# Optimization experiments

Measured on AMD Instinct MI355X. Metric: run time of the kernel, lower is better.

Reference implementation:

```python
import jax, jax.numpy as jnp
import numpy as np

B, D, P, K = 16384, 2048, 64, 5


def setup_inputs() -> dict:
    key = jax.random.key(0)
    k1, k2, k3, k4, k5 = jax.random.split(key, 5)
    s = 1.0 / np.sqrt(D)
    return {
        "x": jax.random.normal(k1, (B, D), dtype=jnp.float32),
        "parent_W": jax.random.normal(k2, (P, D), dtype=jnp.float32) * s,
        "parent_b": jax.random.normal(k3, (P,), dtype=jnp.float32) * s,
        "child_W": jax.random.normal(k4, (P, K, D), dtype=jnp.float32) * s,
        "child_b": jax.random.normal(k5, (P, K), dtype=jnp.float32) * s,
    }


def reference(x, parent_W, parent_b, child_W, child_b):
    # Parent linear: [B, P]
    parent_logits = x @ parent_W.T + parent_b
    # softmax is monotonic, so argmax(softmax(l)) == argmax(l)
    parent_class = jnp.argmax(parent_logits, axis=1)  # [B] int
    # Gather each sample's expert (child classifier) weights: [B, K, D], [B, K]
    Wc = child_W[parent_class]
    bc = child_b[parent_class]
    # Per-sample tiny GEMM, batched: [B, K]
    child_logits = jnp.einsum("bd,bkd->bk", x, Wc) + bc
    return parent_logits, child_logits
```

## Files before the change

kernel.cpp:

```cpp
#include <hip/hip_runtime.h>

#define B_ 16384
#define D_ 2048
#define P_ 64
#define K_ 5

#define BM 64
#define BK 64
#define KS 4
#define KSLICE (D_ / KS)
#define NCH (KSLICE / BK)

__global__ __launch_bounds__(256) void k1_parent(
    const float* __restrict__ x, const float* __restrict__ pW,
    float* __restrict__ part) {
  __shared__ float smem[BK * BM + BK * P_];
  float* xT = smem;
  float* wT = smem + BK * BM;

  const int tid = threadIdx.x;
  const int rt  = blockIdx.x & 255;
  const int ks  = blockIdx.x >> 8;
  const int b0  = rt * BM;
  const int kbase = ks * KSLICE;
  const int q   = tid & 15;
  const int rw  = tid >> 4;
  const int tc4 = (tid & 15) << 2;
  const int tr4 = (tid >> 4) << 2;

  const float* xg = x + (size_t)b0 * D_ + kbase;
  const float* wg = pW + kbase;

  float4 xa[4], wb[4];
#pragma unroll
  for (int j = 0; j < 4; ++j) {
    xa[j] = *(const float4*)&xg[(size_t)(rw + 16 * j) * D_ + (q << 2)];
    wb[j] = *(const float4*)&wg[(size_t)(rw + 16 * j) * D_ + (q << 2)];
  }

  float acc[4][4];
#pragma unroll
  for (int i = 0; i < 4; ++i)
#pragma unroll
    for (int jj = 0; jj < 4; ++jj) acc[i][jj] = 0.f;

  const int swz = q << 2;
  for (int kk = 0; kk < NCH; ++kk) {
#pragma unroll
    for (int j = 0; j < 4; ++j) {
      const int cx = (rw + 16 * j) ^ swz;
      xT[(4 * q + 0) * BM + cx] = xa[j].x;
      xT[(4 * q + 1) * BM + cx] = xa[j].y;
      xT[(4 * q + 2) * BM + cx] = xa[j].z;
      xT[(4 * q + 3) * BM + cx] = xa[j].w;
      wT[(4 * q + 0) * P_ + cx] = wb[j].x;
      wT[(4 * q + 1) * P_ + cx] = wb[j].y;
      wT[(4 * q + 2) * P_ + cx] = wb[j].z;
      wT[(4 * q + 3) * P_ + cx] = wb[j].w;
    }
    __syncthreads();
    if (kk + 1 < NCH) {
      const int d0 = (kk + 1) * BK;
#pragma unroll
      for (int j = 0; j < 4; ++j) {
        xa[j] = *(const float4*)&xg[(size_t)(rw + 16 * j) * D_ + d0 + (q << 2)];
        wb[j] = *(const float4*)&wg[(size_t)(rw + 16 * j) * D_ + d0 + (q << 2)];
      }
    }
#pragma unroll 8
    for (int d = 0; d < BK; ++d) {
      const int sz = ((d >> 2) & 15) << 2;
      const float4 xv = *(const float4*)&xT[d * BM + (tr4 ^ sz)];
      const float4 wv = *(const float4*)&wT[d * P_ + (tc4 ^ sz)];
      acc[0][0] += xv.x * wv.x; acc[0][1] += xv.x * wv.y;
      acc[0][2] += xv.x * wv.z; acc[0][3] += xv.x * wv.w;
      acc[1][0] += xv.y * wv.x; acc[1][1] += xv.y * wv.y;
      acc[1][2] += xv.y * wv.z; acc[1][3] += xv.y * wv.w;
      acc[2][0] += xv.z * wv.x; acc[2][1] += xv.z * wv.y;
      acc[2][2] += xv.z * wv.z; acc[2][3] += xv.z * wv.w;
      acc[3][0] += xv.w * wv.x; acc[3][1] += xv.w * wv.y;
      acc[3][2] += xv.w * wv.z; acc[3][3] += xv.w * wv.w;
    }
    __syncthreads();
  }

  float* po = part + (size_t)ks * (B_ * P_) + (size_t)b0 * P_;
#pragma unroll
  for (int i = 0; i < 4; ++i) {
    float4 v;
    v.x = acc[i][0]; v.y = acc[i][1]; v.z = acc[i][2]; v.w = acc[i][3];
    *(float4*)&po[(size_t)(tr4 + i) * P_ + tc4] = v;
  }
}

__global__ __launch_bounds__(256) void k_reduce(const float* __restrict__ part,
                                                const float* __restrict__ pb,
                                                float* __restrict__ pout,
                                                int* __restrict__ cnt,
                                                int* __restrict__ list) {
  const int wave = threadIdx.x >> 6, lane = threadIdx.x & 63;
  const int r = blockIdx.x * 4 + wave;
  float v = pb[lane];
#pragma unroll
  for (int s = 0; s < KS; ++s)
    v += part[(size_t)s * (B_ * P_) + (size_t)r * P_ + lane];
  pout[(size_t)r * P_ + lane] = v;

  float bv = v;
  int bi = lane;
#pragma unroll
  for (int s = 32; s > 0; s >>= 1) {
    const float ov = __shfl_xor(bv, s, 64);
    const int oi = __shfl_xor(bi, s, 64);
    if (ov > bv || (ov == bv && oi < bi)) { bv = ov; bi = oi; }
  }
  if (lane == 0) {
    const int slot = atomicAdd(&cnt[bi * 16], 1);
    if (slot < 1024) list[bi * 1024 + slot] = r;
  }
}

__global__ __launch_bounds__(256) void k2_child(const float* __restrict__ x,
                                                const float* __restrict__ cW,
                                                const float* __restrict__ cb,
                                                const int* __restrict__ cnt,
                                                const int* __restrict__ list,
                                                float* __restrict__ cout) {
  __shared__ float wlds[K_ * D_];
  const int e   = blockIdx.x >> 2;
  const int chk = blockIdx.x & 3;
  const int tid = threadIdx.x;

  const float4* wg4 = (const float4*)(cW + (size_t)e * (K_ * D_));
  float4* wl4 = (float4*)wlds;
#pragma unroll
  for (int tI = 0; tI < 10; ++tI) wl4[tid + 256 * tI] = wg4[tid + 256 * tI];
  __syncthreads();

  const int n   = min(cnt[e * 16], 1024);
  const int per = (n + 3) >> 2;
  const int lo  = chk * per;
  const int hi  = min(lo + per, n);
  const int m   = hi - lo;
  if (m <= 0) return;

  const int wave = tid >> 6, lane = tid & 63;
  const int wper = (m + 3) >> 2;
  const int wlo  = lo + wave * wper;
  const int whi  = min(wlo + wper, hi);

  const float4* x4 = (const float4*)x;
  const int* mylist = list + e * 1024;

  for (int i0 = wlo; i0 < whi; i0 += 4) {
    const int vb = min(4, whi - i0);
    const int ra = mylist[i0];
    const int rb = mylist[i0 + min(1, vb - 1)];
    const int rc = mylist[i0 + min(2, vb - 1)];
    const int rd = mylist[i0 + min(3, vb - 1)];

    float a[20];
#pragma unroll
    for (int q = 0; q < 20; ++q) a[q] = 0.f;

#pragma unroll
    for (int tt = 0; tt < 8; ++tt) {
      const float4 xv0 = x4[(size_t)ra * 512 + lane + 64 * tt];
      const float4 xv1 = x4[(size_t)rb * 512 + lane + 64 * tt];
      const float4 xv2 = x4[(size_t)rc * 512 + lane + 64 * tt];
      const float4 xv3 = x4[(size_t)rd * 512 + lane + 64 * tt];
#pragma unroll
      for (int k = 0; k < 5; ++k) {
        const float4 wv = wl4[k * 512 + lane + 64 * tt];
        a[0 * 5 + k] += xv0.x * wv.x + xv0.y * wv.y + xv0.z * wv.z + xv0.w * wv.w;
        a[1 * 5 + k] += xv1.x * wv.x + xv1.y * wv.y + xv1.z * wv.z + xv1.w * wv.w;
        a[2 * 5 + k] += xv2.x * wv.x + xv2.y * wv.y + xv2.z * wv.z + xv2.w * wv.w;
        a[3 * 5 + k] += xv3.x * wv.x + xv3.y * wv.y + xv3.z * wv.z + xv3.w * wv.w;
      }
    }
#pragma unroll
    for (int p = 0; p < 10; ++p) {
      float va = a[2 * p], vb2 = a[2 * p + 1];
      va  += __shfl_xor(va, 32, 64);
      vb2 += __shfl_xor(vb2, 32, 64);
      float z = (lane < 32) ? va : vb2;
      z += __shfl_xor(z, 16, 64);
      z += __shfl_xor(z, 8, 64);
      z += __shfl_xor(z, 4, 64);
      z += __shfl_xor(z, 2, 64);
      z += __shfl_xor(z, 1, 64);
      a[2 * p] = z;
    }
    if (lane == 0 || lane == 32) {
      const int off = (lane == 32) ? 1 : 0;
#pragma unroll
      for (int p = 0; p < 10; ++p) {
        const int f = 2 * p + off;
        const int rr = f / 5, kk = f % 5;
        if (rr < vb) {
          const int r = (rr == 0) ? ra : (rr == 1) ? rb : (rr == 2) ? rc : rd;
          cout[(size_t)r * K_ + kk] = a[2 * p] + cb[e * K_ + kk];
        }
      }
    }
  }
}

extern "C" void kernel_launch(void* const* d_in, const int* in_sizes, int n_in,
                              void* d_out, int out_size, void* d_ws, size_t ws_size,
                              hipStream_t stream) {
  const float* x  = (const float*)d_in[0];
  const float* pW = (const float*)d_in[1];
  const float* pb = (const float*)d_in[2];
  const float* cW = (const float*)d_in[3];
  const float* cb = (const float*)d_in[4];
  float* pout = (float*)d_out;
  float* cout = (float*)d_out + (size_t)B_ * P_;

  char* ws = (char*)d_ws;
  int*   cnt  = (int*)ws;
  int*   list = (int*)(ws + 4096);
  float* part = (float*)(ws + 1048576);

  hipMemsetAsync(cnt, 0, 4096, stream);
  k1_parent<<<256 * KS, 256, 0, stream>>>(x, pW, part);
  k_reduce<<<B_ / 4, 256, 0, stream>>>(part, pb, pout, cnt, list);
  k2_child<<<P_ * 4, 256, 0, stream>>>(x, cW, cb, cnt, list, cout);
}
```

Measured before the change: 267.6 us.

## Use split-fp16 MFMA for parent GEMM and fuse bias, argmax, bucketing into it

```diff
diff --git a/kernel.cpp b/kernel.cpp
--- a/kernel.cpp
+++ b/kernel.cpp
@@ -5,118 +5,153 @@
 #define P_ 64
 #define K_ 5
 
-#define BM 64
 #define BK 64
-#define KS 4
-#define KSLICE (D_ / KS)
-#define NCH (KSLICE / BK)
+#define NCH (D_ / BK)
+#define LDR 72
+#define SPLIT_SC 2048.0f
+#define SPLIT_INV (1.0f / 2048.0f)
+
+typedef _Float16 half8 __attribute__((ext_vector_type(8)));
+typedef float f32x4 __attribute__((ext_vector_type(4)));
+
+static __device__ __forceinline__ void split8(const float4 a, const float4 b,
+                                              half8& hi, half8& lo) {
+  const float v[8] = {a.x, a.y, a.z, a.w, b.x, b.y, b.z, b.w};
+#pragma unroll
+  for (int i = 0; i < 8; ++i) {
+    const _Float16 h = (_Float16)v[i];
+    hi[i] = h;
+    lo[i] = (_Float16)((v[i] - (float)h) * SPLIT_SC);
+  }
+}
 
 __global__ __launch_bounds__(256) void k1_parent(
     const float* __restrict__ x, const float* __restrict__ pW,
-    float* __restrict__ part) {
-  __shared__ float smem[BK * BM + BK * P_];
-  float* xT = smem;
-  float* wT = smem + BK * BM;
+    const float* __restrict__ pb, float* __restrict__ pout,
+    int* __restrict__ cnt, int* __restrict__ list) {
+  __shared__ _Float16 xlh[2][64 * LDR], xll[2][64 * LDR];
+  __shared__ _Float16 wlh[2][64 * LDR], wll[2][64 * LDR];
+  __shared__ float rmax[64][4];
+  __shared__ int ridx[64][4];
 
   const int tid = threadIdx.x;
-  const int rt  = blockIdx.x & 255;
-  const int ks  = blockIdx.x >> 8;
-  const int b0  = rt * BM;
-  const int kbase = ks * KSLICE;
-  const int q   = tid & 15;
-  const int rw  = tid >> 4;
-  const int tc4 = (tid & 15) << 2;
-  const int tr4 = (tid >> 4) << 2;
-
-  const float* xg = x + (size_t)b0 * D_ + kbase;
-  const float* wg = pW + kbase;
-
-  float4 xa[4], wb[4];
-#pragma unroll
-  for (int j = 0; j < 4; ++j) {
-    xa[j] = *(const float4*)&xg[(size_t)(rw + 16 * j) * D_ + (q << 2)];
-    wb[j] = *(const float4*)&wg[(size_t)(rw + 16 * j) * D_ + (q << 2)];
-  }
-
-  float acc[4][4];
-#pragma unroll
-  for (int i = 0; i < 4; ++i)
-#pragma unroll
-    for (int jj = 0; jj < 4; ++jj) acc[i][jj] = 0.f;
-
-  const int swz = q << 2;
-  for (int kk = 0; kk < NCH; ++kk) {
+  const int b0 = blockIdx.x * 64;
+  const int w = tid >> 6;
+  const int l = tid & 63;
+  const int r = tid >> 2;
+  const int c = tid & 3;
+
+  const float* xg = x + (size_t)(b0 + r) * D_ + c * 16;
+  const float* wg = pW + (size_t)r * D_ + c * 16;
+  const float bias = pb[w * 16 + (l & 15)];
+
+  const int aoff = (l & 15) * LDR + (l >> 4) * 8;
+  const int boff = (w * 16 + (l & 15)) * LDR + (l >> 4) * 8;
+  const int soff = r * LDR + c * 16;
+
+  f32x4 acc[4], accc[4];
+#pragma unroll
+  for (int fm = 0; fm < 4; ++fm) {
+    acc[fm] = {0.f, 0.f, 0.f, 0.f};
+    accc[fm] = {0.f, 0.f, 0.f, 0.f};
+  }
+
+  {
+    const float4* xp = (const float4*)xg;
+    const float4* wp = (const float4*)wg;
+    half8 h, lo;
+    split8(xp[0], xp[1], h, lo);
+    *(half8*)&xlh[0][soff] = h; *(half8*)&xll[0][soff] = lo;
+    split8(xp[2], xp[3], h, lo);
+    *(half8*)&xlh[0][soff + 8] = h; *(half8*)&xll[0][soff + 8] = lo;
+    split8(wp[0], wp[1], h, lo);
+    *(half8*)&wlh[0][soff] = h; *(half8*)&wll[0][soff] = lo;
+    split8(wp[2], wp[3], h, lo);
+    *(half8*)&wlh[0][soff + 8] = h; *(half8*)&wll[0][soff + 8] = lo;
+  }
+  __syncthreads();
+
+  for (int ch = 0; ch < NCH; ++ch) {
+    const int cur = ch & 1;
+    float4 x0, x1, x2, x3, w0, w1, w2, w3;
+    const bool more = (ch + 1 < NCH);
+    if (more) {
+      const float4* xp = (const float4*)(xg + (ch + 1) * BK);
+      const float4* wp = (const float4*)(wg + (ch + 1) * BK);
+      x0 = xp[0]; x1 = xp[1]; x2 = xp[2]; x3 = xp[3];
+      w0 = wp[0]; w1 = wp[1]; w2 = wp[2]; w3 = wp[3];
+    }
+#pragma unroll
+    for (int s = 0; s < 2; ++s) {
+      const int ko = s * 32;
+      const half8 bh = *(const half8*)&wlh[cur][boff + ko];
+      const half8 bl = *(const half8*)&wll[cur][boff + ko];
+#pragma unroll
+      for (int fm = 0; fm < 4; ++fm) {
+        const half8 ah = *(const half8*)&xlh[cur][aoff + fm * 16 * LDR + ko];
+        const half8 al = *(const half8*)&xll[cur][aoff + fm * 16 * LDR + ko];
+        acc[fm]  = __builtin_amdgcn_mfma_f32_16x16x32_f16(ah, bh, acc[fm], 0, 0, 0);
+        accc[fm] = __builtin_amdgcn_mfma_f32_16x16x32_f16(ah, bl, accc[fm], 0, 0, 0);
+        accc[fm] = __builtin_amdgcn_mfma_f32_16x16x32_f16(al, bh, accc[fm], 0, 0, 0);
+      }
+    }
+    if (more) {
+      const int nxt = cur ^ 1;
+      half8 h, lo;
+      split8(x0, x1, h, lo);
+      *(half8*)&xlh[nxt][soff] = h; *(half8*)&xll[nxt][soff] = lo;
+      split8(x2, x3, h, lo);
+      *(half8*)&xlh[nxt][soff + 8] = h; *(half8*)&xll[nxt][soff + 8] = lo;
+      split8(w0, w1, h, lo);
+      *(half8*)&wlh[nxt][soff] = h; *(half8*)&wll[nxt][soff] = lo;
+      split8(w2, w3, h, lo);
+      *(half8*)&wlh[nxt][soff + 8] = h; *(half8*)&wll[nxt][soff + 8] = lo;
+    }
+    __syncthreads();
+  }
+
+  const int colbase = w * 16 + (l & 15);
+  float val[4][4];
+#pragma unroll
+  for (int fm = 0; fm < 4; ++fm) {
 #pragma unroll
     for (int j = 0; j < 4; ++j) {
-      const int cx = (rw + 16 * j) ^ swz;
-      xT[(4 * q + 0) * BM + cx] = xa[j].x;
-      xT[(4 * q + 1) * BM + cx] = xa[j].y;
-      xT[(4 * q + 2) * BM + cx] = xa[j].z;
-      xT[(4 * q + 3) * BM + cx] = xa[j].w;
-      wT[(4 * q + 0) * P_ + cx] = wb[j].x;
-      wT[(4 * q + 1) * P_ + cx] = wb[j].y;
-      wT[(4 * q + 2) * P_ + cx] = wb[j].z;
-      wT[(4 * q + 3) * P_ + cx] = wb[j].w;
-    }
-    __syncthreads();
-    if (kk + 1 < NCH) {
-      const int d0 = (kk + 1) * BK;
-#pragma unroll
-      for (int j = 0; j < 4; ++j) {
-        xa[j] = *(const float4*)&xg[(size_t)(rw + 16 * j) * D_ + d0 + (q << 2)];
-        wb[j] = *(const float4*)&wg[(size_t)(rw + 16 * j) * D_ + d0 + (q << 2)];
-      }
-    }
-#pragma unroll 8
-    for (int d = 0; d < BK; ++d) {
-      const int sz = ((d >> 2) & 15) << 2;
-      const float4 xv = *(const float4*)&xT[d * BM + (tr4 ^ sz)];
-      const float4 wv = *(const float4*)&wT[d * P_ + (tc4 ^ sz)];
-      acc[0][0] += xv.x * wv.x; acc[0][1] += xv.x * wv.y;
-      acc[0][2] += xv.x * wv.z; acc[0][3] += xv.x * wv.w;
-      acc[1][0] += xv.y * wv.x; acc[1][1] += xv.y * wv.y;
-      acc[1][2] += xv.y * wv.z; acc[1][3] += xv.y * wv.w;
-      acc[2][0] += xv.z * wv.x; acc[2][1] += xv.z * wv.y;
-      acc[2][2] += xv.z * wv.z; acc[2][3] += xv.z * wv.w;
-      acc[3][0] += xv.w * wv.x; acc[3][1] += xv.w * wv.y;
-      acc[3][2] += xv.w * wv.z; acc[3][3] += xv.w * wv.w;
-    }
-    __syncthreads();
-  }
-
-  float* po = part + (size_t)ks * (B_ * P_) + (size_t)b0 * P_;
-#pragma unroll
-  for (int i = 0; i < 4; ++i) {
-    float4 v;
-    v.x = acc[i][0]; v.y = acc[i][1]; v.z = acc[i][2]; v.w = acc[i][3];
-    *(float4*)&po[(size_t)(tr4 + i) * P_ + tc4] = v;
-  }
-}
-
-__global__ __launch_bounds__(256) void k_reduce(const float* __restrict__ part,
-                                                const float* __restrict__ pb,
-                                                float* __restrict__ pout,
-                                                int* __restrict__ cnt,
-                                                int* __restrict__ list) {
-  const int wave = threadIdx.x >> 6, lane = threadIdx.x & 63;
-  const int r = blockIdx.x * 4 + wave;
-  float v = pb[lane];
-#pragma unroll
-  for (int s = 0; s < KS; ++s)
-    v += part[(size_t)s * (B_ * P_) + (size_t)r * P_ + lane];
-  pout[(size_t)r * P_ + lane] = v;
-
-  float bv = v;
-  int bi = lane;
-#pragma unroll
-  for (int s = 32; s > 0; s >>= 1) {
-    const float ov = __shfl_xor(bv, s, 64);
-    const int oi = __shfl_xor(bi, s, 64);
-    if (ov > bv || (ov == bv && oi < bi)) { bv = ov; bi = oi; }
-  }
-  if (lane == 0) {
+      val[fm][j] = acc[fm][j] + accc[fm][j] * SPLIT_INV + bias;
+      const int row = fm * 16 + ((l >> 4) << 2) + j;
+      pout[(size_t)(b0 + row) * P_ + colbase] = val[fm][j];
+    }
+  }
+#pragma unroll
+  for (int fm = 0; fm < 4; ++fm) {
+#pragma unroll
+    for (int j = 0; j < 4; ++j) {
+      float bv = val[fm][j];
+      int bi = colbase;
+#pragma unroll
+      for (int s = 8; s > 0; s >>= 1) {
+        const float ov = __shfl_xor(bv, s, 64);
+        const int oi = __shfl_xor(bi, s, 64);
+        if (ov > bv || (ov == bv && oi < bi)) { bv = ov; bi = oi; }
+      }
+      if ((l & 15) == 0) {
+        const int row = fm * 16 + ((l >> 4) << 2) + j;
+        rmax[row][w] = bv;
+        ridx[row][w] = bi;
+      }
+    }
+  }
+  __syncthreads();
+  if (tid < 64) {
+    float bv = rmax[tid][0];
+    int bi = ridx[tid][0];
+#pragma unroll
+    for (int ww = 1; ww < 4; ++ww) {
+      const float ov = rmax[tid][ww];
+      const int oi = ridx[tid][ww];
+      if (ov > bv || (ov == bv && oi < bi)) { bv = ov; bi = oi; }
+    }
     const int slot = atomicAdd(&cnt[bi * 16], 1);
-    if (slot < 1024) list[bi * 1024 + slot] = r;
+    if (slot < 1024) list[bi * 1024 + slot] = b0 + tid;
   }
 }
 
@@ -127,7 +162,7 @@
                                                 const int* __restrict__ list,
                                                 float* __restrict__ cout) {
   __shared__ float wlds[K_ * D_];
-  const int e   = blockIdx.x >> 2;
+  const int e = blockIdx.x >> 2;
   const int chk = blockIdx.x & 3;
   const int tid = threadIdx.x;
 
@@ -137,17 +172,17 @@
   for (int tI = 0; tI < 10; ++tI) wl4[tid + 256 * tI] = wg4[tid + 256 * tI];
   __syncthreads();
 
-  const int n   = min(cnt[e * 16], 1024);
+  const int n = min(cnt[e * 16], 1024);
   const int per = (n + 3) >> 2;
-  const int lo  = chk * per;
-  const int hi  = min(lo + per, n);
-  const int m   = hi - lo;
+  const int lo = chk * per;
+  const int hi = min(lo + per, n);
+  const int m = hi - lo;
   if (m <= 0) return;
 
   const int wave = tid >> 6, lane = tid & 63;
   const int wper = (m + 3) >> 2;
-  const int wlo  = lo + wave * wper;
-  const int whi  = min(wlo + wper, hi);
+  const int wlo = lo + wave * wper;
+  const int whi = min(wlo + wper, hi);
 
   const float4* x4 = (const float4*)x;
   const int* mylist = list + e * 1024;
@@ -181,7 +216,7 @@
 #pragma unroll
     for (int p = 0; p < 10; ++p) {
       float va = a[2 * p], vb2 = a[2 * p + 1];
-      va  += __shfl_xor(va, 32, 64);
+      va += __shfl_xor(va, 32, 64);
       vb2 += __shfl_xor(vb2, 32, 64);
       float z = (lane < 32) ? va : vb2;
       z += __shfl_xor(z, 16, 64);
@@ -198,8 +233,8 @@
         const int f = 2 * p + off;
         const int rr = f / 5, kk = f % 5;
         if (rr < vb) {
-          const int r = (rr == 0) ? ra : (rr == 1) ? rb : (rr == 2) ? rc : rd;
-          cout[(size_t)r * K_ + kk] = a[2 * p] + cb[e * K_ + kk];
+          const int rX = (rr == 0) ? ra : (rr == 1) ? rb : (rr == 2) ? rc : rd;
+          cout[(size_t)rX * K_ + kk] = a[2 * p] + cb[e * K_ + kk];
         }
       }
     }
@@ -218,12 +253,10 @@
   float* cout = (float*)d_out + (size_t)B_ * P_;
 
   char* ws = (char*)d_ws;
-  int*   cnt  = (int*)ws;
-  int*   list = (int*)(ws + 4096);
-  float* part = (float*)(ws + 1048576);
+  int* cnt  = (int*)ws;
+  int* list = (int*)(ws + 4096);
 
   hipMemsetAsync(cnt, 0, 4096, stream);
-  k1_parent<<<256 * KS, 256, 0, stream>>>(x, pW, part);
-  k_reduce<<<B_ / 4, 256, 0, stream>>>(part, pb, pout, cnt, list);
+  k1_parent<<<B_ / 64, 256, 0, stream>>>(x, pW, pb, pout, cnt, list);
   k2_child<<<P_ * 4, 256, 0, stream>>>(x, cW, cb, cnt, list, cout);
 }
```

Result: no change. 268.9 us (+0.5%).
